# Performance work log

Measured on AMD Instinct MI355X. Metric: run time of the kernel, lower is better.

The kernel has to match this reference:

```python
import jax, jax.numpy as jnp
import numpy as np

B, NUM_FRAMES, NUM_PATCHES = 2, 16, 196
DIM, H, DH = 768, 12, 64
T = NUM_FRAMES * NUM_PATCHES  # 3136
EPS = 1e-5


def setup_inputs() -> dict:
    key = jax.random.key(0)
    ks = jax.random.split(key, 5)
    x = jax.random.normal(ks[0], (B, T, DIM), jnp.float32)
    context = jax.random.normal(ks[1], (B, T, DIM), jnp.float32)
    Wq = jax.random.normal(ks[2], (DIM, H * DH), jnp.float32) * 0.02
    Wkv = jax.random.normal(ks[3], (DIM, 2 * H * DH), jnp.float32) * 0.02
    Wo = jax.random.normal(ks[4], (H * DH, DIM), jnp.float32) * 0.02
    bo = jnp.zeros((DIM,), jnp.float32)
    gamma = jnp.ones((DIM,), jnp.float32)
    beta = jnp.zeros((DIM,), jnp.float32)
    # block-diagonal frame mask: patch i attends to patch j iff same frame
    frame_ids = jnp.arange(T) // NUM_PATCHES
    mask = frame_ids[:, None] == frame_ids[None, :]  # [T, T] bool
    return {"x": x, "context": context, "Wq": Wq, "Wkv": Wkv, "Wo": Wo,
            "bo": bo, "gamma": gamma, "beta": beta, "mask": mask}


def reference(x, context, Wq, Wkv, Wo, bo, gamma, beta, mask):
    # LayerNorm on queries only (torch LN: biased variance, eps=1e-5)
    mu = jnp.mean(x, axis=-1, keepdims=True)
    var = jnp.var(x, axis=-1, keepdims=True)
    xn = (x - mu) * jax.lax.rsqrt(var + EPS) * gamma + beta

    q = xn @ Wq                      # [B, T, H*DH]
    kv = context @ Wkv               # [B, T, 2*H*DH]
    k, v = jnp.split(kv, 2, axis=-1)

    def split_heads(t):
        return t.reshape(B, T, H, DH).transpose(0, 2, 1, 3)  # [B, H, T, DH]

    q, k, v = split_heads(q), split_heads(k), split_heads(v)

    scale = DH ** -0.5
    dots = jnp.einsum('bhnd,bhmd->bhnm', q, k) * scale      # [B, H, T, T]
    dots = jnp.where(mask, dots, -jnp.inf)
    attn = jax.nn.softmax(dots, axis=-1)                    # dropout p=0.0 -> identity
    out = jnp.einsum('bhnm,bhmd->bhnd', attn, v)            # [B, H, T, DH]
    out = out.transpose(0, 2, 1, 3).reshape(B, T, H * DH)
    return out @ Wo + bo
```

## Files before the change

kernel.cpp:

```cpp
#include <hip/hip_runtime.h>
#include <hip/hip_bf16.h>

#define NB 2
#define TT 3136
#define DIM 768
#define NH 12
#define NF 16
#define NP 196

typedef __attribute__((ext_vector_type(8))) short short8;
typedef __attribute__((ext_vector_type(4))) short s16x4;
typedef __attribute__((ext_vector_type(4))) float f32x4;
typedef unsigned int uint;

__device__ __forceinline__ float bf2f(short s) {
    return __uint_as_float(((uint)(unsigned short)s) << 16);
}
__device__ __forceinline__ short f2bs(float f) {
    __hip_bfloat16 h = __float2bfloat16(f);
    short s; __builtin_memcpy(&s, &h, 2); return s;
}
__device__ __forceinline__ void load16_lds(const void* g, void* l) {
    __builtin_amdgcn_global_load_lds(
        (const __attribute__((address_space(1))) unsigned int*)g,
        (__attribute__((address_space(3))) unsigned int*)l, 16, 0, 0);
}

__global__ __launch_bounds__(256)
void prep_w(const float* __restrict__ Wq, const float* __restrict__ Wkv,
            const float* __restrict__ Wo,
            __hip_bfloat16* __restrict__ WqT, __hip_bfloat16* __restrict__ WkvT,
            __hip_bfloat16* __restrict__ WoT) {
    __shared__ float tile[32][33];
    int bx = blockIdx.x;
    const float* W; __hip_bfloat16* WT; int N, n0;
    if (bx < 24)      { W = Wq;  WT = WqT;  N = DIM;     n0 = bx * 32; }
    else if (bx < 72) { W = Wkv; WT = WkvT; N = 2 * DIM; n0 = (bx - 24) * 32; }
    else              { W = Wo;  WT = WoT;  N = DIM;     n0 = (bx - 72) * 32; }
    int k0 = blockIdx.y * 32;
    int tx = threadIdx.x & 31, ty = threadIdx.x >> 5;
#pragma unroll
    for (int i = 0; i < 32; i += 8)
        tile[ty + i][tx] = W[(size_t)(k0 + ty + i) * N + (n0 + tx)];
    __syncthreads();
#pragma unroll
    for (int i = 0; i < 32; i += 8)
        WT[(size_t)(n0 + ty + i) * DIM + (k0 + tx)] = __float2bfloat16(tile[tx][ty + i]);
}

__global__ __launch_bounds__(256)
void prep_xc(const float* __restrict__ ctx, __hip_bfloat16* __restrict__ cb,
             const float* __restrict__ x, const float* __restrict__ gamma,
             const float* __restrict__ beta, __hip_bfloat16* __restrict__ xn) {
    int blk = blockIdx.x, tid = threadIdx.x;
    if (blk < 4704) {
        size_t i = (size_t)blk * 256 + tid;
        f32x4 f; __builtin_memcpy(&f, ctx + i * 4, 16);
        s16x4 s;
#pragma unroll
        for (int j = 0; j < 4; j++) s[j] = f2bs(f[j]);
        __builtin_memcpy((short*)cb + i * 4, &s, 8);
        return;
    }
    int row = blk - 4704;
    const float* xr = x + (size_t)row * DIM;
    float v[3], s = 0.f, ss = 0.f;
#pragma unroll
    for (int i = 0; i < 3; i++) {
        v[i] = xr[tid + i * 256];
        s += v[i]; ss += v[i] * v[i];
    }
#pragma unroll
    for (int off = 32; off; off >>= 1) {
        s += __shfl_xor(s, off);
        ss += __shfl_xor(ss, off);
    }
    __shared__ float red[8];
    int wid = tid >> 6, lane = tid & 63;
    if (lane == 0) { red[wid] = s; red[wid + 4] = ss; }
    __syncthreads();
    if (tid == 0) {
        float S = red[0] + red[1] + red[2] + red[3];
        float SS = red[4] + red[5] + red[6] + red[7];
        float mu = S / DIM;
        float var = SS / DIM - mu * mu;
        red[0] = mu;
        red[1] = rsqrtf(var + 1e-5f);
    }
    __syncthreads();
    float mu = red[0], rs = red[1];
#pragma unroll
    for (int i = 0; i < 3; i++) {
        int c = tid + i * 256;
        xn[(size_t)row * DIM + c] = __float2bfloat16((v[i] - mu) * rs * gamma[c] + beta[c]);
    }
}

__global__ __launch_bounds__(512, 1)
void gemm_qkv(const __hip_bfloat16* __restrict__ xn,
              const __hip_bfloat16* __restrict__ cb,
              const __hip_bfloat16* __restrict__ WqT,
              const __hip_bfloat16* __restrict__ WkvT,
              __hip_bfloat16* __restrict__ qbuf,
              __hip_bfloat16* __restrict__ kvbuf) {
    __shared__ short lds[2][2][2][8192];

    int orig = blockIdx.x;
    int xcd = orig & 7, pos = orig >> 3;
    int wgid = (xcd < 1 ? xcd * 29 : 29 + (xcd - 1) * 28) + pos;
    int mt = wgid / 9, nt = wgid - mt * 9;

    const __hip_bfloat16 *Abase, *Bbase; __hip_bfloat16* Cbase;
    int N, n0;
    if (nt < 3) { Abase = xn; Bbase = WqT;  Cbase = qbuf;  N = DIM;  n0 = nt * 256; }
    else        { Abase = cb; Bbase = WkvT; Cbase = kvbuf; N = 1536; n0 = (nt - 3) * 256; }
    int m0 = mt * 256;

    int tid = threadIdx.x, lane = tid & 63, wave = tid >> 6;
    int r = lane & 15, q = lane >> 4;
    int wm = wave >> 2, wn = wave & 3;
    f32x4 acc[8][4] = {};

    auto stageK = [&](int buf, int kt) {
        int k0 = kt * 64;
#pragma unroll
        for (int h = 0; h < 2; h++)
#pragma unroll
            for (int s = 0; s < 2; s++) {
                int idx = s * 512 + tid;
                int row = idx >> 3, cg = idx & 7;
                int w = (cg << 4) ^ ((row & 7) << 4);
                int grow = m0 + h * 128 + row;
                if (grow > TT * NB - 1) grow = TT * NB - 1;
                load16_lds((const char*)Abase + ((size_t)grow * DIM + k0) * 2 + w,
                           (char*)&lds[buf][0][h][0] + idx * 16);
            }
#pragma unroll
        for (int h = 0; h < 2; h++)
#pragma unroll
            for (int s = 0; s < 2; s++) {
                int idx = s * 512 + tid;
                int row = idx >> 3, cg = idx & 7;
                int w = (cg << 4) ^ ((row & 7) << 4);
                int grow = n0 + h * 128 + row;
                load16_lds((const char*)Bbase + ((size_t)grow * DIM + k0) * 2 + w,
                           (char*)&lds[buf][1][h][0] + idx * 16);
            }
    };

    auto read_frag = [&](const char* base, int frag, int ks) {
        short8 v;
        int row_ = frag * 16 + r;
        int byte_ = row_ * 128 + ((ks * 64 + q * 16) ^ ((r & 7) << 4));
        __builtin_memcpy(&v, base + byte_, 16);
        return v;
    };

    stageK(0, 0);
    asm volatile("s_waitcnt vmcnt(0)" ::: "memory");
    __builtin_amdgcn_s_barrier();

    for (int t = 0; t < 12; ++t) {
        int cur = t & 1;
        const char* Ah = (const char*)&lds[cur][0][wm][0];
        const char* Bh = (const char*)&lds[cur][1][wn >> 1][0];
        int bbase = (wn & 1) * 4;
        short8 breg[4][2];
#pragma unroll
        for (int p = 0; p < 4; p++) {
            short8 areg[2][2];
#pragma unroll
            for (int i = 0; i < 2; i++)
#pragma unroll
                for (int ks = 0; ks < 2; ks++)
                    areg[i][ks] = read_frag(Ah, p * 2 + i, ks);
            if (p == 0) {
#pragma unroll
                for (int n = 0; n < 4; n++)
#pragma unroll
                    for (int ks = 0; ks < 2; ks++)
                        breg[n][ks] = read_frag(Bh, bbase + n, ks);
                if (t < 11) stageK(cur ^ 1, t + 1);
            }
            __builtin_amdgcn_s_barrier();
            __builtin_amdgcn_s_setprio(1);
#pragma unroll
            for (int i = 0; i < 2; i++)
#pragma unroll
                for (int n = 0; n < 4; n++)
#pragma unroll
                    for (int ks = 0; ks < 2; ks++)
                        acc[p * 2 + i][n] = __builtin_amdgcn_mfma_f32_16x16x32_bf16(
                            areg[i][ks], breg[n][ks], acc[p * 2 + i][n], 0, 0, 0);
            __builtin_amdgcn_s_setprio(0);
            if (p == 3)
                asm volatile("s_waitcnt vmcnt(0)" ::: "memory");
            __builtin_amdgcn_s_barrier();
        }
    }

#pragma unroll
    for (int mf = 0; mf < 8; mf++)
#pragma unroll
        for (int n = 0; n < 4; n++)
#pragma unroll
            for (int rr = 0; rr < 4; rr++) {
                int row = m0 + wm * 128 + mf * 16 + q * 4 + rr;
                if (row < TT * NB) {
                    int col = n0 + wn * 64 + n * 16 + r;
                    Cbase[(size_t)row * N + col] = __float2bfloat16(acc[mf][n][rr]);
                }
            }
}

__global__ __launch_bounds__(256)
void gemm_o(const __hip_bfloat16* __restrict__ A,
            const __hip_bfloat16* __restrict__ BT,
            const float* __restrict__ bias,
            float* __restrict__ C) {
    __shared__ short sA[2][128 * 64];
    __shared__ short sB[2][128 * 64];
    int orig = blockIdx.x;
    int xcd = orig & 7, pos = orig >> 3;
    int wgid = (xcd < 6 ? xcd * 37 : 222 + (xcd - 6) * 36) + pos;
    int mt = wgid / 6, nt = wgid - mt * 6;
    int m0 = mt * 128, n0 = nt * 128;
    int tid = threadIdx.x, lane = tid & 63, wave = tid >> 6;
    int r = lane & 15, q = lane >> 4;
    int wm = (wave & 1) * 64, wn = (wave >> 1) * 64;
    f32x4 acc[4][4] = {};

    auto stage = [&](int buf, int k0) {
#pragma unroll
        for (int i = 0; i < 4; i++) {
            int c = i * 256 + tid;
            int row = c >> 3, cg = c & 7;
            load16_lds(A + (size_t)(m0 + row) * DIM + k0 + cg * 8, &sA[buf][c * 8]);
        }
#pragma unroll
        for (int i = 0; i < 4; i++) {
            int c = i * 256 + tid;
            int row = c >> 3, cg = c & 7;
            load16_lds(BT + (size_t)(n0 + row) * DIM + k0 + cg * 8, &sB[buf][c * 8]);
        }
    };
    auto compute = [&](int buf) {
#pragma unroll
        for (int ks = 0; ks < 2; ks++) {
            short8 af[4], bfv[4];
#pragma unroll
            for (int t = 0; t < 4; t++) {
                __builtin_memcpy(&af[t],  &sA[buf][(wm + t * 16 + r) * 64 + ks * 32 + q * 8], 16);
                __builtin_memcpy(&bfv[t], &sB[buf][(wn + t * 16 + r) * 64 + ks * 32 + q * 8], 16);
            }
            __builtin_amdgcn_s_setprio(1);
#pragma unroll
            for (int mi = 0; mi < 4; mi++)
#pragma unroll
                for (int ni = 0; ni < 4; ni++)
                    acc[mi][ni] = __builtin_amdgcn_mfma_f32_16x16x32_bf16(
                        af[mi], bfv[ni], acc[mi][ni], 0, 0, 0);
            __builtin_amdgcn_s_setprio(0);
        }
    };

    stage(0, 0);
    __syncthreads();
    int cur = 0;
#pragma unroll 2
    for (int t = 0; t < 11; ++t) {
        stage(cur ^ 1, (t + 1) * 64);
        compute(cur);
        __syncthreads();
        cur ^= 1;
    }
    compute(cur);

    float bv[4];
#pragma unroll
    for (int ni = 0; ni < 4; ni++) bv[ni] = bias[n0 + wn + ni * 16 + r];
#pragma unroll
    for (int mi = 0; mi < 4; mi++)
#pragma unroll
        for (int ni = 0; ni < 4; ni++)
#pragma unroll
            for (int rr = 0; rr < 4; rr++) {
                int row = m0 + wm + mi * 16 + q * 4 + rr;
                int col = n0 + wn + ni * 16 + r;
                C[(size_t)row * DIM + col] = acc[mi][ni][rr] + bv[ni];
            }
}

__global__ __launch_bounds__(448)
void attn_kernel(__hip_bfloat16* qo,
                 const __hip_bfloat16* __restrict__ kvb) {
    __shared__ short sQ[112 * 66];
    __shared__ short sK[208 * 66];
    __shared__ short sVT[64 * 226];
    int blk = blockIdx.x;
    int half = blk & 1;
    int rest = blk >> 1;
    int f = rest % NF, h = (rest / NF) % NH, b = rest / (NF * NH);
    size_t tok0 = (size_t)b * TT + (size_t)f * NP;
    int row0 = half * 98;
    int tid = threadIdx.x, wave = tid >> 6, lane = tid & 63;
    int r = lane & 15, q = lane >> 4;

    for (int e = tid; e < 896; e += 448) {
        int row = e >> 3, cg = e & 7;
        short8 t = {0,0,0,0,0,0,0,0};
        if (row < 98)
            __builtin_memcpy(&t, qo + (tok0 + row0 + row) * DIM + h * 64 + cg * 8, 16);
        __builtin_memcpy(&sQ[row * 66 + cg * 8], &t, 16);
    }
    for (int e = tid; e < 1664; e += 448) {
        int row = e >> 3, cg = e & 7;
        short8 t = {0,0,0,0,0,0,0,0};
        if (row < NP)
            __builtin_memcpy(&t, kvb + (tok0 + row) * 1536 + h * 64 + cg * 8, 16);
        __builtin_memcpy(&sK[row * 66 + cg * 8], &t, 16);
    }
    for (int jj = 0; jj < 224; jj += 28) {
        int j = jj + (tid >> 4);
        int d = (tid & 15) * 4;
        s16x4 v = {0, 0, 0, 0};
        if (j < NP)
            __builtin_memcpy(&v, kvb + (tok0 + j) * 1536 + DIM + h * 64 + d, 8);
#pragma unroll
        for (int i = 0; i < 4; i++) sVT[(d + i) * 226 + j] = v[i];
    }
    __syncthreads();

    f32x4 sacc[13];
    short8 qf0, qf1;
    __builtin_memcpy(&qf0, &sQ[(wave * 16 + r) * 66 + q * 8], 16);
    __builtin_memcpy(&qf1, &sQ[(wave * 16 + r) * 66 + 32 + q * 8], 16);
#pragma unroll
    for (int jf = 0; jf < 13; jf++) {
        f32x4 a = {};
        short8 kf;
        __builtin_memcpy(&kf, &sK[(jf * 16 + r) * 66 + q * 8], 16);
        a = __builtin_amdgcn_mfma_f32_16x16x32_bf16(kf, qf0, a, 0, 0, 0);
        __builtin_memcpy(&kf, &sK[(jf * 16 + r) * 66 + 32 + q * 8], 16);
        a = __builtin_amdgcn_mfma_f32_16x16x32_bf16(kf, qf1, a, 0, 0, 0);
        sacc[jf] = a;
    }

    const float scale = 0.125f;
    float mx = -INFINITY;
#pragma unroll
    for (int jf = 0; jf < 13; jf++)
#pragma unroll
        for (int rg = 0; rg < 4; rg++) {
            bool valid = (jf < 12) | (q == 0);
            if (valid) mx = fmaxf(mx, sacc[jf][rg] * scale);
        }
    mx = fmaxf(mx, __shfl_xor(mx, 16));
    mx = fmaxf(mx, __shfl_xor(mx, 32));
    float ps = 0.f;
#pragma unroll
    for (int jf = 0; jf < 13; jf++)
#pragma unroll
        for (int rg = 0; rg < 4; rg++) {
            bool valid = (jf < 12) | (q == 0);
            float p = valid ? __expf(sacc[jf][rg] * scale - mx) : 0.f;
            sacc[jf][rg] = p;
            ps += p;
        }
    ps += __shfl_xor(ps, 16);
    ps += __shfl_xor(ps, 32);
    float inv = 1.f / ps;

    int srcl[8];
#pragma unroll
    for (int e = 0; e < 8; e++)
        srcl[e] = ((((q * 8 + e) >> 2) & 3) << 4) | r;
    short8 pa[7];
#pragma unroll
    for (int c = 0; c < 7; c++) {
#pragma unroll
        for (int e = 0; e < 8; e++) {
            float v0 = __shfl(sacc[2 * c][e & 3], srcl[e], 64);
            float v1 = (c < 6) ? __shfl(sacc[2 * c + 1][e & 3], srcl[e], 64) : 0.f;
            float val = (q >= 2) ? v1 : v0;
            pa[c][e] = f2bs(val * inv);
        }
    }

#pragma unroll
    for (int nt = 0; nt < 4; nt++) {
        f32x4 oacc = {};
#pragma unroll
        for (int kc = 0; kc < 7; kc++) {
            short8 bfv;
            __builtin_memcpy(&bfv, &sVT[(nt * 16 + r) * 226 + kc * 32 + q * 8], 16);
            oacc = __builtin_amdgcn_mfma_f32_16x16x32_bf16(pa[kc], bfv, oacc, 0, 0, 0);
        }
#pragma unroll
        for (int rg = 0; rg < 4; rg++) {
            int local = wave * 16 + q * 4 + rg;
            if (local < 98)
                qo[(tok0 + row0 + local) * DIM + h * 64 + nt * 16 + r] =
                    __float2bfloat16(oacc[rg]);
        }
    }
}

extern "C" void kernel_launch(void* const* d_in, const int* in_sizes, int n_in,
                              void* d_out, int out_size, void* d_ws, size_t ws_size,
                              hipStream_t stream) {
    const float* x     = (const float*)d_in[0];
    const float* ctx   = (const float*)d_in[1];
    const float* Wq    = (const float*)d_in[2];
    const float* Wkv   = (const float*)d_in[3];
    const float* Wo    = (const float*)d_in[4];
    const float* bo    = (const float*)d_in[5];
    const float* gamma = (const float*)d_in[6];
    const float* beta  = (const float*)d_in[7];

    char* ws = (char*)d_ws;
    __hip_bfloat16* cbuf  = (__hip_bfloat16*)(ws + 0);
    __hip_bfloat16* kvbuf = (__hip_bfloat16*)(ws + 9633792);
    __hip_bfloat16* qbuf  = (__hip_bfloat16*)(ws + 28901376);
    __hip_bfloat16* WqT   = (__hip_bfloat16*)(ws + 38535168);
    __hip_bfloat16* WkvT  = (__hip_bfloat16*)(ws + 39714816);
    __hip_bfloat16* WoT   = (__hip_bfloat16*)(ws + 42074112);
    __hip_bfloat16* xnbuf = (__hip_bfloat16*)d_out;
    float*          out   = (float*)d_out;

    prep_w<<<dim3(96, 24), 256, 0, stream>>>(Wq, Wkv, Wo, WqT, WkvT, WoT);
    prep_xc<<<10976, 256, 0, stream>>>(ctx, cbuf, x, gamma, beta, xnbuf);
    gemm_qkv<<<225, 512, 0, stream>>>(xnbuf, cbuf, WqT, WkvT, qbuf, kvbuf);
    attn_kernel<<<NB * NH * NF * 2, 448, 0, stream>>>(qbuf, kvbuf);
    gemm_o<<<294, 256, 0, stream>>>(qbuf, WoT, bo, out);
}
```

Measured before the change: 202.1 us.

## Fuse prep kernels, wave-per-row LayerNorm, one attention block per frame-head, packed shuffles

Merges the weight-transpose and input-conversion/LayerNorm kernels into one launch, removing a launch gap. LayerNorm now uses one wave per row with vectorized loads and no LDS reduction or barriers. The attention kernel handles both query halves of a frame-head in one block, so K and V are staged once instead of twice. The probability redistribution now shuffles packed bf16 pairs, which halves the shuffle count. The cost is half as many attention blocks (384), each doing twice the work serially, which may leave the GPU underfilled.

```diff
diff --git a/kernel.cpp b/kernel.cpp
--- a/kernel.cpp
+++ b/kernel.cpp
@@ -20,6 +20,9 @@
     __hip_bfloat16 h = __float2bfloat16(f);
     short s; __builtin_memcpy(&s, &h, 2); return s;
 }
+__device__ __forceinline__ uint pack2bf(float a, float b) {
+    return (uint)(unsigned short)f2bs(a) | ((uint)(unsigned short)f2bs(b) << 16);
+}
 __device__ __forceinline__ void load16_lds(const void* g, void* l) {
     __builtin_amdgcn_global_load_lds(
         (const __attribute__((address_space(1))) unsigned int*)g,
@@ -27,32 +30,33 @@
 }
 
 __global__ __launch_bounds__(256)
-void prep_w(const float* __restrict__ Wq, const float* __restrict__ Wkv,
-            const float* __restrict__ Wo,
-            __hip_bfloat16* __restrict__ WqT, __hip_bfloat16* __restrict__ WkvT,
-            __hip_bfloat16* __restrict__ WoT) {
+void prep_all(const float* __restrict__ Wq, const float* __restrict__ Wkv,
+              const float* __restrict__ Wo,
+              __hip_bfloat16* __restrict__ WqT, __hip_bfloat16* __restrict__ WkvT,
+              __hip_bfloat16* __restrict__ WoT,
+              const float* __restrict__ ctx, __hip_bfloat16* __restrict__ cb,
+              const float* __restrict__ x, const float* __restrict__ gamma,
+              const float* __restrict__ beta, __hip_bfloat16* __restrict__ xn) {
     __shared__ float tile[32][33];
-    int bx = blockIdx.x;
-    const float* W; __hip_bfloat16* WT; int N, n0;
-    if (bx < 24)      { W = Wq;  WT = WqT;  N = DIM;     n0 = bx * 32; }
-    else if (bx < 72) { W = Wkv; WT = WkvT; N = 2 * DIM; n0 = (bx - 24) * 32; }
-    else              { W = Wo;  WT = WoT;  N = DIM;     n0 = (bx - 72) * 32; }
-    int k0 = blockIdx.y * 32;
-    int tx = threadIdx.x & 31, ty = threadIdx.x >> 5;
-#pragma unroll
-    for (int i = 0; i < 32; i += 8)
-        tile[ty + i][tx] = W[(size_t)(k0 + ty + i) * N + (n0 + tx)];
-    __syncthreads();
-#pragma unroll
-    for (int i = 0; i < 32; i += 8)
-        WT[(size_t)(n0 + ty + i) * DIM + (k0 + tx)] = __float2bfloat16(tile[tx][ty + i]);
-}
-
-__global__ __launch_bounds__(256)
-void prep_xc(const float* __restrict__ ctx, __hip_bfloat16* __restrict__ cb,
-             const float* __restrict__ x, const float* __restrict__ gamma,
-             const float* __restrict__ beta, __hip_bfloat16* __restrict__ xn) {
     int blk = blockIdx.x, tid = threadIdx.x;
+    if (blk < 2304) {
+        int bx = blk % 96, ky = blk / 96;
+        const float* W; __hip_bfloat16* WT; int N, n0;
+        if (bx < 24)      { W = Wq;  WT = WqT;  N = DIM;     n0 = bx * 32; }
+        else if (bx < 72) { W = Wkv; WT = WkvT; N = 2 * DIM; n0 = (bx - 24) * 32; }
+        else              { W = Wo;  WT = WoT;  N = DIM;     n0 = (bx - 72) * 32; }
+        int k0 = ky * 32;
+        int tx = tid & 31, ty = tid >> 5;
+#pragma unroll
+        for (int i = 0; i < 32; i += 8)
+            tile[ty + i][tx] = W[(size_t)(k0 + ty + i) * N + (n0 + tx)];
+        __syncthreads();
+#pragma unroll
+        for (int i = 0; i < 32; i += 8)
+            WT[(size_t)(n0 + ty + i) * DIM + (k0 + tx)] = __float2bfloat16(tile[tx][ty + i]);
+        return;
+    }
+    blk -= 2304;
     if (blk < 4704) {
         size_t i = (size_t)blk * 256 + tid;
         f32x4 f; __builtin_memcpy(&f, ctx + i * 4, 16);
@@ -62,37 +66,35 @@
         __builtin_memcpy((short*)cb + i * 4, &s, 8);
         return;
     }
-    int row = blk - 4704;
+    blk -= 4704;
+    int wave = tid >> 6, lane = tid & 63;
+    int row = blk * 4 + wave;
     const float* xr = x + (size_t)row * DIM;
-    float v[3], s = 0.f, ss = 0.f;
+    f32x4 v[3];
+    float s = 0.f, ss = 0.f;
 #pragma unroll
     for (int i = 0; i < 3; i++) {
-        v[i] = xr[tid + i * 256];
-        s += v[i]; ss += v[i] * v[i];
+        __builtin_memcpy(&v[i], xr + lane * 4 + i * 256, 16);
+#pragma unroll
+        for (int j = 0; j < 4; j++) { s += v[i][j]; ss += v[i][j] * v[i][j]; }
     }
 #pragma unroll
     for (int off = 32; off; off >>= 1) {
         s += __shfl_xor(s, off);
         ss += __shfl_xor(ss, off);
     }
-    __shared__ float red[8];
-    int wid = tid >> 6, lane = tid & 63;
-    if (lane == 0) { red[wid] = s; red[wid + 4] = ss; }
-    __syncthreads();
-    if (tid == 0) {
-        float S = red[0] + red[1] + red[2] + red[3];
-        float SS = red[4] + red[5] + red[6] + red[7];
-        float mu = S / DIM;
-        float var = SS / DIM - mu * mu;
-        red[0] = mu;
-        red[1] = rsqrtf(var + 1e-5f);
-    }
-    __syncthreads();
-    float mu = red[0], rs = red[1];
+    float mu = s / DIM;
+    float rs = rsqrtf(ss / DIM - mu * mu + 1e-5f);
 #pragma unroll
     for (int i = 0; i < 3; i++) {
-        int c = tid + i * 256;
-        xn[(size_t)row * DIM + c] = __float2bfloat16((v[i] - mu) * rs * gamma[c] + beta[c]);
+        int c = lane * 4 + i * 256;
+        f32x4 g, bt;
+        __builtin_memcpy(&g, gamma + c, 16);
+        __builtin_memcpy(&bt, beta + c, 16);
+        s16x4 o;
+#pragma unroll
+        for (int j = 0; j < 4; j++) o[j] = f2bs((v[i][j] - mu) * rs * g[j] + bt[j]);
+        __builtin_memcpy((short*)xn + (size_t)row * DIM + c, &o, 8);
     }
 }
 
@@ -294,23 +296,20 @@
 __global__ __launch_bounds__(448)
 void attn_kernel(__hip_bfloat16* qo,
                  const __hip_bfloat16* __restrict__ kvb) {
-    __shared__ short sQ[112 * 66];
+    __shared__ short sQ[210 * 66];
     __shared__ short sK[208 * 66];
     __shared__ short sVT[64 * 226];
     int blk = blockIdx.x;
-    int half = blk & 1;
-    int rest = blk >> 1;
-    int f = rest % NF, h = (rest / NF) % NH, b = rest / (NF * NH);
+    int f = blk % NF, h = (blk / NF) % NH, b = blk / (NF * NH);
     size_t tok0 = (size_t)b * TT + (size_t)f * NP;
-    int row0 = half * 98;
     int tid = threadIdx.x, wave = tid >> 6, lane = tid & 63;
     int r = lane & 15, q = lane >> 4;
 
-    for (int e = tid; e < 896; e += 448) {
+    for (int e = tid; e < 1680; e += 448) {
         int row = e >> 3, cg = e & 7;
         short8 t = {0,0,0,0,0,0,0,0};
-        if (row < 98)
-            __builtin_memcpy(&t, qo + (tok0 + row0 + row) * DIM + h * 64 + cg * 8, 16);
+        if (row < NP)
+            __builtin_memcpy(&t, qo + (tok0 + row) * DIM + h * 64 + cg * 8, 16);
         __builtin_memcpy(&sQ[row * 66 + cg * 8], &t, 16);
     }
     for (int e = tid; e < 1664; e += 448) {
@@ -331,77 +330,92 @@
     }
     __syncthreads();
 
-    f32x4 sacc[13];
-    short8 qf0, qf1;
-    __builtin_memcpy(&qf0, &sQ[(wave * 16 + r) * 66 + q * 8], 16);
-    __builtin_memcpy(&qf1, &sQ[(wave * 16 + r) * 66 + 32 + q * 8], 16);
-#pragma unroll
-    for (int jf = 0; jf < 13; jf++) {
-        f32x4 a = {};
-        short8 kf;
-        __builtin_memcpy(&kf, &sK[(jf * 16 + r) * 66 + q * 8], 16);
-        a = __builtin_amdgcn_mfma_f32_16x16x32_bf16(kf, qf0, a, 0, 0, 0);
-        __builtin_memcpy(&kf, &sK[(jf * 16 + r) * 66 + 32 + q * 8], 16);
-        a = __builtin_amdgcn_mfma_f32_16x16x32_bf16(kf, qf1, a, 0, 0, 0);
-        sacc[jf] = a;
-    }
-
-    const float scale = 0.125f;
-    float mx = -INFINITY;
-#pragma unroll
-    for (int jf = 0; jf < 13; jf++)
-#pragma unroll
-        for (int rg = 0; rg < 4; rg++) {
-            bool valid = (jf < 12) | (q == 0);
-            if (valid) mx = fmaxf(mx, sacc[jf][rg] * scale);
-        }
-    mx = fmaxf(mx, __shfl_xor(mx, 16));
-    mx = fmaxf(mx, __shfl_xor(mx, 32));
-    float ps = 0.f;
-#pragma unroll
-    for (int jf = 0; jf < 13; jf++)
-#pragma unroll
-        for (int rg = 0; rg < 4; rg++) {
-            bool valid = (jf < 12) | (q == 0);
-            float p = valid ? __expf(sacc[jf][rg] * scale - mx) : 0.f;
-            sacc[jf][rg] = p;
-            ps += p;
-        }
-    ps += __shfl_xor(ps, 16);
-    ps += __shfl_xor(ps, 32);
-    float inv = 1.f / ps;
-
-    int srcl[8];
-#pragma unroll
-    for (int e = 0; e < 8; e++)
-        srcl[e] = ((((q * 8 + e) >> 2) & 3) << 4) | r;
-    short8 pa[7];
-#pragma unroll
-    for (int c = 0; c < 7; c++) {
-#pragma unroll
-        for (int e = 0; e < 8; e++) {
-            float v0 = __shfl(sacc[2 * c][e & 3], srcl[e], 64);
-            float v1 = (c < 6) ? __shfl(sacc[2 * c + 1][e & 3], srcl[e], 64) : 0.f;
-            float val = (q >= 2) ? v1 : v0;
-            pa[c][e] = f2bs(val * inv);
-        }
-    }
-
-#pragma unroll
-    for (int nt = 0; nt < 4; nt++) {
-        f32x4 oacc = {};
-#pragma unroll
-        for (int kc = 0; kc < 7; kc++) {
-            short8 bfv;
-            __builtin_memcpy(&bfv, &sVT[(nt * 16 + r) * 226 + kc * 32 + q * 8], 16);
-            oacc = __builtin_amdgcn_mfma_f32_16x16x32_bf16(pa[kc], bfv, oacc, 0, 0, 0);
-        }
-#pragma unroll
-        for (int rg = 0; rg < 4; rg++) {
-            int local = wave * 16 + q * 4 + rg;
-            if (local < 98)
-                qo[(tok0 + row0 + local) * DIM + h * 64 + nt * 16 + r] =
-                    __float2bfloat16(oacc[rg]);
+    for (int half = 0; half < 2; half++) {
+        int row0 = half * 98;
+
+        f32x4 sacc[13];
+        short8 qf0, qf1;
+        __builtin_memcpy(&qf0, &sQ[(row0 + wave * 16 + r) * 66 + q * 8], 16);
+        __builtin_memcpy(&qf1, &sQ[(row0 + wave * 16 + r) * 66 + 32 + q * 8], 16);
+#pragma unroll
+        for (int jf = 0; jf < 13; jf++) {
+            f32x4 a = {};
+            short8 kf;
+            __builtin_memcpy(&kf, &sK[(jf * 16 + r) * 66 + q * 8], 16);
+            a = __builtin_amdgcn_mfma_f32_16x16x32_bf16(kf, qf0, a, 0, 0, 0);
+            __builtin_memcpy(&kf, &sK[(jf * 16 + r) * 66 + 32 + q * 8], 16);
+            a = __builtin_amdgcn_mfma_f32_16x16x32_bf16(kf, qf1, a, 0, 0, 0);
+            sacc[jf] = a;
+        }
+
+        const float scale = 0.125f;
+        float mx = -INFINITY;
+#pragma unroll
+        for (int jf = 0; jf < 13; jf++)
+#pragma unroll
+            for (int rg = 0; rg < 4; rg++) {
+                bool valid = (jf < 12) | (q == 0);
+                if (valid) mx = fmaxf(mx, sacc[jf][rg] * scale);
+            }
+        mx = fmaxf(mx, __shfl_xor(mx, 16));
+        mx = fmaxf(mx, __shfl_xor(mx, 32));
+        float ps = 0.f;
+#pragma unroll
+        for (int jf = 0; jf < 13; jf++)
+#pragma unroll
+            for (int rg = 0; rg < 4; rg++) {
+                bool valid = (jf < 12) | (q == 0);
+                float p = valid ? __expf(sacc[jf][rg] * scale - mx) : 0.f;
+                sacc[jf][rg] = p;
+                ps += p;
+            }
+        ps += __shfl_xor(ps, 16);
+        ps += __shfl_xor(ps, 32);
+        float inv = 1.f / ps;
+
+        uint pk01[13], pk23[13];
+#pragma unroll
+        for (int jf = 0; jf < 13; jf++) {
+            pk01[jf] = pack2bf(sacc[jf][0] * inv, sacc[jf][1] * inv);
+            pk23[jf] = pack2bf(sacc[jf][2] * inv, sacc[jf][3] * inv);
+        }
+        int sl = (((2 * q) & 3) << 4) | r;
+        int sh = (((2 * q + 1) & 3) << 4) | r;
+        bool hiq = q >= 2;
+        short8 pa[7];
+#pragma unroll
+        for (int c = 0; c < 7; c++) {
+            uint a0 = (uint)__shfl((int)pk01[2 * c], sl, 64);
+            uint a1 = (uint)__shfl((int)pk23[2 * c], sl, 64);
+            uint a2 = (uint)__shfl((int)pk01[2 * c], sh, 64);
+            uint a3 = (uint)__shfl((int)pk23[2 * c], sh, 64);
+            uint b0 = 0, b1 = 0, b2 = 0, b3 = 0;
+            if (c < 6) {
+                b0 = (uint)__shfl((int)pk01[2 * c + 1], sl, 64);
+                b1 = (uint)__shfl((int)pk23[2 * c + 1], sl, 64);
+                b2 = (uint)__shfl((int)pk01[2 * c + 1], sh, 64);
+                b3 = (uint)__shfl((int)pk23[2 * c + 1], sh, 64);
+            }
+            uint w[4] = { hiq ? b0 : a0, hiq ? b1 : a1, hiq ? b2 : a2, hiq ? b3 : a3 };
+            __builtin_memcpy(&pa[c], w, 16);
+        }
+
+#pragma unroll
+        for (int nt = 0; nt < 4; nt++) {
+            f32x4 oacc = {};
+#pragma unroll
+            for (int kc = 0; kc < 7; kc++) {
+                short8 bfv;
+                __builtin_memcpy(&bfv, &sVT[(nt * 16 + r) * 226 + kc * 32 + q * 8], 16);
+                oacc = __builtin_amdgcn_mfma_f32_16x16x32_bf16(pa[kc], bfv, oacc, 0, 0, 0);
+            }
+#pragma unroll
+            for (int rg = 0; rg < 4; rg++) {
+                int local = wave * 16 + q * 4 + rg;
+                if (local < 98)
+                    qo[(tok0 + row0 + local) * DIM + h * 64 + nt * 16 + r] =
+                        __float2bfloat16(oacc[rg]);
+            }
         }
     }
 }
@@ -428,9 +442,9 @@
     __hip_bfloat16* xnbuf = (__hip_bfloat16*)d_out;
     float*          out   = (float*)d_out;
 
-    prep_w<<<dim3(96, 24), 256, 0, stream>>>(Wq, Wkv, Wo, WqT, WkvT, WoT);
-    prep_xc<<<10976, 256, 0, stream>>>(ctx, cbuf, x, gamma, beta, xnbuf);
+    prep_all<<<8576, 256, 0, stream>>>(Wq, Wkv, Wo, WqT, WkvT, WoT,
+                                       ctx, cbuf, x, gamma, beta, xnbuf);
     gemm_qkv<<<225, 512, 0, stream>>>(xnbuf, cbuf, WqT, WkvT, qbuf, kvbuf);
-    attn_kernel<<<NB * NH * NF * 2, 448, 0, stream>>>(qbuf, kvbuf);
+    attn_kernel<<<NB * NH * NF, 448, 0, stream>>>(qbuf, kvbuf);
     gemm_o<<<294, 256, 0, stream>>>(qbuf, WoT, bo, out);
 }
```

Result: slower. 213.0 us (+5.4%).
